# Kernel tuning notes

Hardware: AMD Instinct MI355X
Metric: run time of the kernel (lower is better)

## Reference

```python
import jax, jax.numpy as jnp
import numpy as np

N_NODES = 50000
N_EDGES = 800000
IN_DIM = 128
HID_DIM = 64
OUT_DIM = 40
N_REL = 8


def setup_inputs() -> dict:
    key = jax.random.key(0)
    ks = jax.random.split(key, 12)
    x = jax.random.normal(ks[0], (N_NODES, IN_DIM), dtype=jnp.float32)
    edge_index = jax.random.randint(ks[1], (2, N_EDGES), 0, N_NODES, dtype=jnp.int64)
    edge_type = jax.random.randint(ks[2], (N_EDGES,), 0, N_REL, dtype=jnp.int64)
    s = 0.05
    W1 = jax.random.normal(ks[3], (N_REL, IN_DIM, HID_DIM), dtype=jnp.float32) * s
    root1 = jax.random.normal(ks[4], (IN_DIM, HID_DIM), dtype=jnp.float32) * s
    b1 = jnp.zeros((HID_DIM,), dtype=jnp.float32)
    W2 = jax.random.normal(ks[5], (N_REL, HID_DIM, HID_DIM), dtype=jnp.float32) * s
    root2 = jax.random.normal(ks[6], (HID_DIM, HID_DIM), dtype=jnp.float32) * s
    b2 = jnp.zeros((HID_DIM,), dtype=jnp.float32)
    Wl = jax.random.normal(ks[7], (HID_DIM, OUT_DIM), dtype=jnp.float32) * s
    bl = jnp.zeros((OUT_DIM,), dtype=jnp.float32)
    return {"x": x, "edge_index": edge_index, "edge_type": edge_type,
            "W1": W1, "root1": root1, "b1": b1,
            "W2": W2, "root2": root2, "b2": b2,
            "Wl": Wl, "bl": bl}


def _rgcn_conv(x, W, Wroot, b, src, dst, edge_type):
    # PyG RGCNConv (no bases/blocks, aggr='mean'):
    #   out[i] = sum_r mean_{(j->i) of rel r} (x[j] @ W[r]) + x[i] @ Wroot + b
    N = x.shape[0]
    R = W.shape[0]
    h = jnp.einsum('ni,rio->rno', x, W)        # [R, N, out]
    msgs = h[edge_type, src]                   # [E, out] edge gather
    seg = edge_type * N + dst                  # per (relation, dst) segment
    sums = jax.ops.segment_sum(msgs, seg, num_segments=R * N)
    cnt = jax.ops.segment_sum(jnp.ones((msgs.shape[0],), x.dtype), seg,
                              num_segments=R * N)
    mean = sums / jnp.maximum(cnt, 1.0)[:, None]
    agg = mean.reshape(R, N, -1).sum(axis=0)   # sum over relations
    return agg + x @ Wroot + b


def reference(x, edge_index, edge_type, W1, root1, b1, W2, root2, b2, Wl, bl):
    src, dst = edge_index[0], edge_index[1]
    h = jax.nn.relu(_rgcn_conv(x, W1, root1, b1, src, dst, edge_type))
    # dropout is identity in eval mode
    h = jax.nn.relu(_rgcn_conv(h, W2, root2, b2, src, dst, edge_type))
    logits = h @ Wl + bl
    return jax.nn.log_softmax(logits, axis=1)
```

## Files before the change

### kernel.cpp

```cpp
#include <hip/hip_runtime.h>
#include <hip/hip_bf16.h>
#include <cmath>


#define IN_DIM 128
#define HID 64
#define OUT_DIM 40
#define NREL 8
#define NCOLS 576
#define CAP 64
#define CSTR 16

typedef __attribute__((ext_vector_type(8))) short short8;
typedef __attribute__((ext_vector_type(4))) short short4v;
typedef __attribute__((ext_vector_type(4))) float floatx4;
typedef __attribute__((ext_vector_type(2))) float f32x2;

static __device__ __forceinline__ short f2bf(float f) {
  __hip_bfloat16 h = __float2bfloat16(f);
  return __builtin_bit_cast(short, h);
}
static __device__ __forceinline__ float bflo(unsigned int u) {
  return __int_as_float(u << 16);
}
static __device__ __forceinline__ float bfhi(unsigned int u) {
  return __int_as_float(u & 0xffff0000u);
}
static __device__ __forceinline__ unsigned int packbf(float x, float y) {
  unsigned int lo = (unsigned short)f2bf(x);
  unsigned int hi = (unsigned short)f2bf(y);
  return lo | (hi << 16);
}

__global__ void pack_bt(const float* __restrict__ W1, const float* __restrict__ root1,
                        short* __restrict__ Bt1,
                        const float* __restrict__ W2, const float* __restrict__ root2,
                        short* __restrict__ Bt2,
                        int* __restrict__ cursor, int nzero4) {
  const int PB1 = (NCOLS * IN_DIM + 255) / 256;
  const int PB2 = (NCOLS * HID + 255) / 256;
  int b = blockIdx.x;
  if (b < PB1) {
    int i = b * 256 + threadIdx.x;
    if (i >= NCOLS * IN_DIM) return;
    int c = i / IN_DIM, k = i % IN_DIM;
    float v = (c < NREL * HID)
      ? W1[((size_t)(c >> 6) * IN_DIM + k) * HID + (c & 63)]
      : root1[(size_t)k * HID + (c - NREL * HID)];
    Bt1[i] = f2bf(v);
  } else if (b < PB1 + PB2) {
    int i = (b - PB1) * 256 + threadIdx.x;
    if (i >= NCOLS * HID) return;
    int c = i / HID, k = i % HID;
    float v = (c < NREL * HID)
      ? W2[((size_t)(c >> 6) * HID + k) * HID + (c & 63)]
      : root2[(size_t)k * HID + (c - NREL * HID)];
    Bt2[i] = f2bf(v);
  } else {
    int i = (b - PB1 - PB2) * 256 + threadIdx.x;
    if (i < nzero4) {
      int4 z; z.x = 0; z.y = 0; z.z = 0; z.w = 0;
      ((int4*)cursor)[i] = z;
    }
  }
}

template<int K, int AMODE>
__device__ __forceinline__ void gemm_dev(
    short* As, short* Bs,
    const void* __restrict__ Aptr, const short* __restrict__ Bt,
    const float* __restrict__ bias, short* __restrict__ H,
    unsigned short* __restrict__ AGG, int M, int row0)
{
  constexpr int AST = K + 8;
  constexpr int CB = K / 8;
  constexpr int NCH = 64 * CB / 256;
  int tid = threadIdx.x;
  int wv = tid >> 6, lane = tid & 63;
  int lm = lane & 15, quad = lane >> 4;

  int bn[NCH], bko[NCH];
  #pragma unroll
  for (int j = 0; j < NCH; ++j) {
    int i = tid + j * 256;
    bn[j] = i / CB; bko[j] = i % CB;
  }

  short8 breg[NCH];
  #pragma unroll
  for (int j = 0; j < NCH; ++j)
    breg[j] = *(const short8*)(Bt + (unsigned)(bn[j] * K + bko[j] * 8));

  if (AMODE == 0) {
    const float* A = (const float*)Aptr;
    constexpr int CH = K / 4;
    for (int i = tid; i < 64 * CH; i += 256) {
      int r = i / CH, kq = i % CH;
      int gr = row0 + r; if (gr >= M) gr = M - 1;
      float4 v = *(const float4*)(A + (unsigned)(gr * K + kq * 4));
      short4v s;
      s.x = f2bf(v.x); s.y = f2bf(v.y); s.z = f2bf(v.z); s.w = f2bf(v.w);
      *(short4v*)(As + r * AST + kq * 4) = s;
    }
  } else {
    const short* A = (const short*)Aptr;
    constexpr int CH = K / 8;
    for (int i = tid; i < 64 * CH; i += 256) {
      int r = i / CH, ko = i % CH;
      int gr = row0 + r; if (gr >= M) gr = M - 1;
      short8 v = *(const short8*)(A + (unsigned)(gr * K + ko * 8));
      #pragma unroll
      for (int j = 0; j < 8; ++j)
        if ((unsigned short)v[j] & 0x8000u) v[j] = 0;
      *(short8*)(As + r * AST + ko * 8) = v;
    }
  }

  const short* ap = As + (16 * wv + lm) * AST + quad * 8;
  int rowg = row0 + 16 * wv + lm;

  for (int cy = 0; cy < 9; ++cy) {
    #pragma unroll
    for (int j = 0; j < NCH; ++j)
      *(short8*)(Bs + bn[j] * AST + bko[j] * 8) = breg[j];
    __syncthreads();

    if (cy < 8) {
      #pragma unroll
      for (int j = 0; j < NCH; ++j)
        breg[j] = *(const short8*)(
            Bt + (unsigned)(((cy + 1) * 64 + bn[j]) * K + bko[j] * 8));
    }

    floatx4 acc[4] = {{0,0,0,0},{0,0,0,0},{0,0,0,0},{0,0,0,0}};
    #pragma unroll
    for (int ks = 0; ks < K / 32; ++ks) {
      short8 a = *(const short8*)(ap + ks * 32);
      #pragma unroll
      for (int nb = 0; nb < 4; ++nb) {
        short8 b = *(const short8*)(Bs + (nb * 16 + lm) * AST + ks * 32 + quad * 8);
        acc[nb] = __builtin_amdgcn_mfma_f32_16x16x32_bf16(b, a, acc[nb], 0, 0, 0);
      }
    }
    __syncthreads();

    if (cy < 8) {
      if (rowg < M) {
        short* hrow = H + (unsigned)rowg * (NREL * HID) + cy * 64 + quad * 4;
        #pragma unroll
        for (int nb = 0; nb < 4; ++nb) {
          short4v s;
          s.x = f2bf(acc[nb][0]); s.y = f2bf(acc[nb][1]);
          s.z = f2bf(acc[nb][2]); s.w = f2bf(acc[nb][3]);
          *(short4v*)(hrow + nb * 16) = s;
        }
      }
    } else {
      if (rowg < M) {
        unsigned short* arow = AGG + (unsigned)rowg * HID + quad * 4;
        #pragma unroll
        for (int nb = 0; nb < 4; ++nb) {
          float4 bv = *(const float4*)(bias + nb * 16 + quad * 4);
          short4v s;
          s.x = f2bf(acc[nb][0] + bv.x); s.y = f2bf(acc[nb][1] + bv.y);
          s.z = f2bf(acc[nb][2] + bv.z); s.w = f2bf(acc[nb][3] + bv.w);
          *(short4v*)(arow + nb * 16) = s;
        }
      }
    }
  }
}

__global__ __launch_bounds__(256, 4) void gemm1_scatter(
    const float* __restrict__ A, const short* __restrict__ Bt,
    const float* __restrict__ bias, short* __restrict__ H,
    unsigned short* __restrict__ AGG, int M, int SB,
    const int* __restrict__ src, const int* __restrict__ dst,
    const int* __restrict__ et,
    int* __restrict__ cursor, int* __restrict__ ev, int E)
{
  constexpr int AST = IN_DIM + 8;
  __shared__ short As[64 * AST];
  __shared__ short Bs[64 * AST];
  if ((int)blockIdx.x >= SB) {
    gemm_dev<IN_DIM, 0>(As, Bs, A, Bt, bias, H, AGG, M, (blockIdx.x - SB) * 64);
  } else {
    int e = blockIdx.x * 256 + threadIdx.x;
    if (e >= E) return;
    int d = dst[e];
    int pos = atomicAdd(&cursor[d * CSTR], 1);
    if (pos < CAP)
      __builtin_nontemporal_store((src[e] << 3) | et[e], &ev[d * CAP + pos]);
  }
}

__global__ __launch_bounds__(256, 4) void gemm2_mfma(
    const unsigned short* __restrict__ A, const short* __restrict__ Bt,
    const float* __restrict__ bias, short* __restrict__ H,
    unsigned short* __restrict__ AGG, int M)
{
  constexpr int AST = HID + 8;
  __shared__ short As[64 * AST];
  __shared__ short Bs[64 * AST];
  gemm_dev<HID, 1>(As, Bs, A, Bt, bias, H, AGG, M, blockIdx.x * 64);
}

static __device__ __forceinline__ void agg_dst(
    const uint2* __restrict__ Hu2, const int* __restrict__ evr,
    int4 e0, int4 e1, int4 e2, int4 e3,
    int cnt, int qloc, int sub, int lhl, int h,
    float& a0, float& a1, float& a2, float& a3)
{
  int vv0[8] = {e0.x, e0.y, e0.z, e0.w, e1.x, e1.y, e1.z, e1.w};
  int vv1[8] = {e2.x, e2.y, e2.z, e2.w, e3.x, e3.y, e3.z, e3.w};
  int base0 = qloc * 8, base1 = 16 + qloc * 8;
  uint2 hv[8];

  #pragma unroll
  for (int i = 0; i < 8; ++i) {
    bool ok = (base0 + i) < cnt;
    int v = ok ? vv0[i] : 0;
    hv[i] = Hu2[(unsigned)v * 16u + (unsigned)sub];
  }

  int myrel = lhl & 7;
  int c = 0;
  #pragma unroll
  for (int i = 0; i < 8; ++i)
    c += ((base0 + i) < cnt && (vv0[i] & 7) == myrel) ? 1 : 0;
  #pragma unroll
  for (int i = 0; i < 8; ++i)
    c += ((base1 + i) < cnt && (vv1[i] & 7) == myrel) ? 1 : 0;
  c += __shfl_xor(c, 16, 64);
  if (cnt > 32) {
    int eu = evr[32 + lhl];
    bool valid = (32 + lhl) < cnt;
    unsigned long long hm = 0xffffffffull << (h * 32);
    int rr = eu & 7;
    #pragma unroll
    for (int r = 0; r < 8; ++r) {
      unsigned long long m = __ballot(valid && rr == r);
      int cr = __popcll(m & hm);
      if (myrel == r) c += cr;
    }
  }
  float wreg = (c > 0) ? (1.0f / (float)c) : 0.0f;

  f32x2 A01 = {a0, a1}, A23 = {a2, a3};
  #pragma unroll
  for (int i = 0; i < 8; ++i) {
    bool ok = (base0 + i) < cnt;
    float w0 = __shfl(wreg, h * 32 + (vv0[i] & 7), 64);
    float w = ok ? w0 : 0.f;
    f32x2 w2 = {w, w};
    f32x2 h01 = {bflo(hv[i].x), bfhi(hv[i].x)};
    f32x2 h23 = {bflo(hv[i].y), bfhi(hv[i].y)};
    A01 += h01 * w2;
    A23 += h23 * w2;
  }
  if (cnt > 16) {
    #pragma unroll
    for (int i = 0; i < 8; ++i) {
      bool ok = (base1 + i) < cnt;
      int v = ok ? vv1[i] : 0;
      hv[i] = Hu2[(unsigned)v * 16u + (unsigned)sub];
    }
    #pragma unroll
    for (int i = 0; i < 8; ++i) {
      bool ok = (base1 + i) < cnt;
      float w0 = __shfl(wreg, h * 32 + (vv1[i] & 7), 64);
      float w = ok ? w0 : 0.f;
      f32x2 w2 = {w, w};
      f32x2 h01 = {bflo(hv[i].x), bfhi(hv[i].x)};
      f32x2 h23 = {bflo(hv[i].y), bfhi(hv[i].y)};
      A01 += h01 * w2;
      A23 += h23 * w2;
    }
  }
  if (cnt > 32) {
    #pragma unroll
    for (int P = 2; P < 4; ++P) {
      if (cnt > P * 16) {
        const int4* pp = (const int4*)(evr + P * 16 + qloc * 8);
        int4 f0 = pp[0], f1 = pp[1];
        int vv[8] = {f0.x, f0.y, f0.z, f0.w, f1.x, f1.y, f1.z, f1.w};
        int bs = P * 16 + qloc * 8;
        #pragma unroll
        for (int i = 0; i < 8; ++i) {
          bool ok = (bs + i) < cnt;
          int v = ok ? vv[i] : 0;
          hv[i] = Hu2[(unsigned)v * 16u + (unsigned)sub];
        }
        #pragma unroll
        for (int i = 0; i < 8; ++i) {
          bool ok = (bs + i) < cnt;
          float w0 = __shfl(wreg, h * 32 + (vv[i] & 7), 64);
          float w = ok ? w0 : 0.f;
          f32x2 w2 = {w, w};
          f32x2 h01 = {bflo(hv[i].x), bfhi(hv[i].x)};
          f32x2 h23 = {bflo(hv[i].y), bfhi(hv[i].y)};
          A01 += h01 * w2;
          A23 += h23 * w2;
        }
      }
    }
  }
  a0 = A01.x; a1 = A01.y; a2 = A23.x; a3 = A23.y;
  a0 += __shfl_xor(a0, 16, 64);
  a1 += __shfl_xor(a1, 16, 64);
  a2 += __shfl_xor(a2, 16, 64);
  a3 += __shfl_xor(a3, 16, 64);
}

__global__ __launch_bounds__(256) void csr_agg(
    const short* __restrict__ H, const int* __restrict__ cursor,
    const int* __restrict__ ev, unsigned short* __restrict__ AGG, int N)
{
  int tid = threadIdx.x;
  int wv = tid >> 6, lane = tid & 63;
  int h = lane >> 5, lhl = lane & 31, qloc = lhl >> 4, sub = lhl & 15;
  int d = blockIdx.x * 8 + wv * 2 + h;
  int dc = d < N ? d : N - 1;

  int cnt = cursor[dc * CSTR];
  const int* evr = ev + dc * CAP;
  const int4* p0 = (const int4*)(evr + qloc * 8);
  int4 e0 = p0[0], e1 = p0[1];
  const int4* p1 = (const int4*)(evr + 16 + qloc * 8);
  int4 e2 = p1[0], e3 = p1[1];
  uint2* aggrow = (uint2*)(AGG + (size_t)dc * HID);
  uint2 iv = {0, 0};
  if (qloc == 0) iv = aggrow[sub];
  if (cnt > CAP) cnt = CAP;

  float a0 = 0.f, a1 = 0.f, a2 = 0.f, a3 = 0.f;
  if (qloc == 0) {
    a0 = bflo(iv.x); a1 = bfhi(iv.x); a2 = bflo(iv.y); a3 = bfhi(iv.y);
  }
  agg_dst((const uint2*)H, evr, e0, e1, e2, e3, cnt, qloc, sub, lhl, h,
          a0, a1, a2, a3);
  if (d < N && qloc == 0) {
    uint2 ov;
    ov.x = packbf(a0, a1);
    ov.y = packbf(a2, a3);
    aggrow[sub] = ov;
  }
}

__global__ __launch_bounds__(256) void csr_agg_final(
    const short* __restrict__ H, const int* __restrict__ cursor,
    const int* __restrict__ ev, const unsigned short* __restrict__ AGG,
    const float* __restrict__ Wl, const float* __restrict__ bl,
    float* __restrict__ out, int N)
{
  __shared__ float sWl[HID * OUT_DIM];
  __shared__ float sbl[OUT_DIM];
  __shared__ float sh[8][HID];
  int tid = threadIdx.x;
  int wv = tid >> 6, lane = tid & 63;
  int h = lane >> 5, lhl = lane & 31, qloc = lhl >> 4, sub = lhl & 15;
  int d = blockIdx.x * 8 + wv * 2 + h;
  int dc = d < N ? d : N - 1;

  int cnt = cursor[dc * CSTR];
  const int* evr = ev + dc * CAP;
  const int4* p0 = (const int4*)(evr + qloc * 8);
  int4 e0 = p0[0], e1 = p0[1];
  const int4* p1 = (const int4*)(evr + 16 + qloc * 8);
  int4 e2 = p1[0], e3 = p1[1];
  uint2 iv = ((const uint2*)(AGG + (size_t)dc * HID))[sub];
  if (cnt > CAP) cnt = CAP;

  float a0 = 0.f, a1 = 0.f, a2 = 0.f, a3 = 0.f;
  if (qloc == 0) {
    a0 = bflo(iv.x); a1 = bfhi(iv.x); a2 = bflo(iv.y); a3 = bfhi(iv.y);
  }
  agg_dst((const uint2*)H, evr, e0, e1, e2, e3, cnt, qloc, sub, lhl, h,
          a0, a1, a2, a3);
  if (qloc == 0) {
    float4 v;
    v.x = fmaxf(a0, 0.f); v.y = fmaxf(a1, 0.f);
    v.z = fmaxf(a2, 0.f); v.w = fmaxf(a3, 0.f);
    *(float4*)(&sh[wv * 2 + h][4 * sub]) = v;
  }

  for (int i = tid; i < HID * OUT_DIM; i += 256) sWl[i] = Wl[i];
  if (tid < OUT_DIM) sbl[tid] = bl[tid];
  __syncthreads();

  #pragma unroll
  for (int ii = 0; ii < 2; ++ii) {
    int dd = blockIdx.x * 8 + wv * 2 + ii;
    const float* row = sh[wv * 2 + ii];
    float logit = -__builtin_inff();
    if (lane < OUT_DIM) {
      float t = sbl[lane];
      #pragma unroll 8
      for (int k = 0; k < HID; ++k) t += row[k] * sWl[k * OUT_DIM + lane];
      logit = t;
    }
    float m = logit;
    #pragma unroll
    for (int o = 32; o > 0; o >>= 1) m = fmaxf(m, __shfl_xor(m, o, 64));
    float ex = (lane < OUT_DIM) ? expf(logit - m) : 0.f;
    float s = ex;
    #pragma unroll
    for (int o = 32; o > 0; o >>= 1) s += __shfl_xor(s, o, 64);
    if (dd < N && lane < OUT_DIM)
      out[(size_t)dd * OUT_DIM + lane] = logit - m - logf(s);
  }
}

extern "C" void kernel_launch(void* const* d_in, const int* in_sizes, int n_in,
                              void* d_out, int out_size, void* d_ws, size_t ws_size,
                              hipStream_t stream) {
  const float* x     = (const float*)d_in[0];
  const int*   eidx  = (const int*)d_in[1];
  const int*   etype = (const int*)d_in[2];
  const float* W1    = (const float*)d_in[3];
  const float* root1 = (const float*)d_in[4];
  const float* b1    = (const float*)d_in[5];
  const float* W2    = (const float*)d_in[6];
  const float* root2 = (const float*)d_in[7];
  const float* b2    = (const float*)d_in[8];
  const float* Wl    = (const float*)d_in[9];
  const float* bl    = (const float*)d_in[10];

  int N = in_sizes[0] / IN_DIM;
  int E = in_sizes[2];
  const int* srcp = eidx;
  const int* dstp = eidx + E;

  char* ws = (char*)d_ws;
  size_t off = 0;
  auto alloc = [&](size_t bytes) -> char* {
    char* p = ws + off;
    off += (bytes + 255) & ~(size_t)255;
    return p;
  };
  short* Bt1    = (short*)alloc((size_t)NCOLS * IN_DIM * 2);
  short* Bt2    = (short*)alloc((size_t)NCOLS * HID * 2);
  int*   cursor = (int*)alloc((size_t)N * CSTR * 4);
  int*   ev     = (int*)alloc((size_t)N * CAP * 4);
  short* H1     = (short*)alloc((size_t)N * NREL * HID * 2);
  short* H2     = (short*)alloc((size_t)N * NREL * HID * 2);
  unsigned short* AGG1 = (unsigned short*)alloc((size_t)N * HID * 2);
  unsigned short* AGG2 = (unsigned short*)alloc((size_t)N * HID * 2);

  const int PB1 = (NCOLS * IN_DIM + 255) / 256;
  const int PB2 = (NCOLS * HID + 255) / 256;
  int nzero4 = (N * CSTR) / 4;
  int ZB = (nzero4 + 255) / 256;
  pack_bt<<<PB1 + PB2 + ZB, 256, 0, stream>>>(W1, root1, Bt1, W2, root2, Bt2,
                                              cursor, nzero4);

  int GB = (N + 63) / 64;
  int SB = (E + 255) / 256;
  gemm1_scatter<<<SB + GB, 256, 0, stream>>>(x, Bt1, b1, H1, AGG1, N, SB,
                                             srcp, dstp, etype, cursor, ev, E);

  csr_agg<<<(N + 7) / 8, 256, 0, stream>>>(H1, cursor, ev, AGG1, N);

  gemm2_mfma<<<GB, 256, 0, stream>>>(AGG1, Bt2, b2, H2, AGG2, N);

  csr_agg_final<<<(N + 7) / 8, 256, 0, stream>>>(H2, cursor, ev, AGG2,
                                                 Wl, bl, (float*)d_out, N);
}
```

Baseline: 266.4 us.

## Fuse layer-1 aggregation with layer-2 GEMM through shared memory

Merges the layer-1 CSR aggregation kernel and the layer-2 MFMA GEMM into one kernel. Each block aggregates 64 destination rows, applies ReLU, and writes them as bf16 straight into the GEMM's shared-memory A tile, so the AGG1 round trip through global memory and one launch go away. It also reorders gemm1_scatter so GEMM blocks come before scatter blocks in the grid. The cost is fewer concurrently active warps during aggregation (one block of 256 threads handles 64 rows serially in 8 reps) and more shared-memory pressure in the fused kernel.

```diff
diff --git a/kernel.cpp b/kernel.cpp
--- a/kernel.cpp
+++ b/kernel.cpp
@@ -91,7 +91,7 @@
   for (int j = 0; j < NCH; ++j)
     breg[j] = *(const short8*)(Bt + (unsigned)(bn[j] * K + bko[j] * 8));
 
-  if (AMODE == 0) {
+  if constexpr (AMODE == 0) {
     const float* A = (const float*)Aptr;
     constexpr int CH = K / 4;
     for (int i = tid; i < 64 * CH; i += 256) {
@@ -102,7 +102,7 @@
       s.x = f2bf(v.x); s.y = f2bf(v.y); s.z = f2bf(v.z); s.w = f2bf(v.w);
       *(short4v*)(As + r * AST + kq * 4) = s;
     }
-  } else {
+  } else if constexpr (AMODE == 1) {
     const short* A = (const short*)Aptr;
     constexpr int CH = K / 8;
     for (int i = tid; i < 64 * CH; i += 256) {
@@ -174,7 +174,7 @@
 __global__ __launch_bounds__(256, 4) void gemm1_scatter(
     const float* __restrict__ A, const short* __restrict__ Bt,
     const float* __restrict__ bias, short* __restrict__ H,
-    unsigned short* __restrict__ AGG, int M, int SB,
+    unsigned short* __restrict__ AGG, int M, int GB,
     const int* __restrict__ src, const int* __restrict__ dst,
     const int* __restrict__ et,
     int* __restrict__ cursor, int* __restrict__ ev, int E)
@@ -182,27 +182,16 @@
   constexpr int AST = IN_DIM + 8;
   __shared__ short As[64 * AST];
   __shared__ short Bs[64 * AST];
-  if ((int)blockIdx.x >= SB) {
-    gemm_dev<IN_DIM, 0>(As, Bs, A, Bt, bias, H, AGG, M, (blockIdx.x - SB) * 64);
+  if ((int)blockIdx.x < GB) {
+    gemm_dev<IN_DIM, 0>(As, Bs, A, Bt, bias, H, AGG, M, blockIdx.x * 64);
   } else {
-    int e = blockIdx.x * 256 + threadIdx.x;
+    int e = (blockIdx.x - GB) * 256 + threadIdx.x;
     if (e >= E) return;
     int d = dst[e];
     int pos = atomicAdd(&cursor[d * CSTR], 1);
     if (pos < CAP)
       __builtin_nontemporal_store((src[e] << 3) | et[e], &ev[d * CAP + pos]);
   }
-}
-
-__global__ __launch_bounds__(256, 4) void gemm2_mfma(
-    const unsigned short* __restrict__ A, const short* __restrict__ Bt,
-    const float* __restrict__ bias, short* __restrict__ H,
-    unsigned short* __restrict__ AGG, int M)
-{
-  constexpr int AST = HID + 8;
-  __shared__ short As[64 * AST];
-  __shared__ short Bs[64 * AST];
-  gemm_dev<HID, 1>(As, Bs, A, Bt, bias, H, AGG, M, blockIdx.x * 64);
 }
 
 static __device__ __forceinline__ void agg_dst(
@@ -312,39 +301,50 @@
   a3 += __shfl_xor(a3, 16, 64);
 }
 
-__global__ __launch_bounds__(256) void csr_agg(
-    const short* __restrict__ H, const int* __restrict__ cursor,
-    const int* __restrict__ ev, unsigned short* __restrict__ AGG, int N)
+__global__ __launch_bounds__(256) void agg_gemm2(
+    const short* __restrict__ H1, const int* __restrict__ cursor,
+    const int* __restrict__ ev, const unsigned short* __restrict__ AGG1,
+    const short* __restrict__ Bt2, const float* __restrict__ bias2,
+    short* __restrict__ H2, unsigned short* __restrict__ AGG2, int N)
 {
+  constexpr int AST = HID + 8;
+  __shared__ short As[64 * AST];
+  __shared__ short Bs[64 * AST];
   int tid = threadIdx.x;
   int wv = tid >> 6, lane = tid & 63;
   int h = lane >> 5, lhl = lane & 31, qloc = lhl >> 4, sub = lhl & 15;
-  int d = blockIdx.x * 8 + wv * 2 + h;
-  int dc = d < N ? d : N - 1;
-
-  int cnt = cursor[dc * CSTR];
-  const int* evr = ev + dc * CAP;
-  const int4* p0 = (const int4*)(evr + qloc * 8);
-  int4 e0 = p0[0], e1 = p0[1];
-  const int4* p1 = (const int4*)(evr + 16 + qloc * 8);
-  int4 e2 = p1[0], e3 = p1[1];
-  uint2* aggrow = (uint2*)(AGG + (size_t)dc * HID);
-  uint2 iv = {0, 0};
-  if (qloc == 0) iv = aggrow[sub];
-  if (cnt > CAP) cnt = CAP;
-
-  float a0 = 0.f, a1 = 0.f, a2 = 0.f, a3 = 0.f;
-  if (qloc == 0) {
-    a0 = bflo(iv.x); a1 = bfhi(iv.x); a2 = bflo(iv.y); a3 = bfhi(iv.y);
-  }
-  agg_dst((const uint2*)H, evr, e0, e1, e2, e3, cnt, qloc, sub, lhl, h,
-          a0, a1, a2, a3);
-  if (d < N && qloc == 0) {
-    uint2 ov;
-    ov.x = packbf(a0, a1);
-    ov.y = packbf(a2, a3);
-    aggrow[sub] = ov;
-  }
+  int hw = wv * 2 + h;
+  int row0 = blockIdx.x * 64;
+
+  for (int rep = 0; rep < 8; ++rep) {
+    int dloc = hw * 8 + rep;
+    int d = row0 + dloc;
+    int dc = d < N ? d : N - 1;
+
+    int cnt = cursor[dc * CSTR];
+    const int* evr = ev + dc * CAP;
+    const int4* p0 = (const int4*)(evr + qloc * 8);
+    int4 e0 = p0[0], e1 = p0[1];
+    const int4* p1 = (const int4*)(evr + 16 + qloc * 8);
+    int4 e2 = p1[0], e3 = p1[1];
+    uint2 iv = {0, 0};
+    if (qloc == 0) iv = ((const uint2*)(AGG1 + (size_t)dc * HID))[sub];
+    if (cnt > CAP) cnt = CAP;
+
+    float a0 = 0.f, a1 = 0.f, a2 = 0.f, a3 = 0.f;
+    if (qloc == 0) {
+      a0 = bflo(iv.x); a1 = bfhi(iv.x); a2 = bflo(iv.y); a3 = bfhi(iv.y);
+    }
+    agg_dst((const uint2*)H1, evr, e0, e1, e2, e3, cnt, qloc, sub, lhl, h,
+            a0, a1, a2, a3);
+    if (qloc == 0) {
+      short4v s;
+      s.x = f2bf(fmaxf(a0, 0.f)); s.y = f2bf(fmaxf(a1, 0.f));
+      s.z = f2bf(fmaxf(a2, 0.f)); s.w = f2bf(fmaxf(a3, 0.f));
+      *(short4v*)(As + dloc * AST + 4 * sub) = s;
+    }
+  }
+  gemm_dev<HID, 2>(As, Bs, nullptr, Bt2, bias2, H2, AGG2, N, row0);
 }
 
 __global__ __launch_bounds__(256) void csr_agg_final(
@@ -456,12 +456,11 @@
 
   int GB = (N + 63) / 64;
   int SB = (E + 255) / 256;
-  gemm1_scatter<<<SB + GB, 256, 0, stream>>>(x, Bt1, b1, H1, AGG1, N, SB,
+  gemm1_scatter<<<GB + SB, 256, 0, stream>>>(x, Bt1, b1, H1, AGG1, N, GB,
                                              srcp, dstp, etype, cursor, ev, E);
 
-  csr_agg<<<(N + 7) / 8, 256, 0, stream>>>(H1, cursor, ev, AGG1, N);
-
-  gemm2_mfma<<<GB, 256, 0, stream>>>(AGG1, Bt2, b2, H2, AGG2, N);
+  agg_gemm2<<<GB, 256, 0, stream>>>(H1, cursor, ev, AGG1, Bt2, b2,
+                                    H2, AGG2, N);
 
   csr_agg_final<<<(N + 7) / 8, 256, 0, stream>>>(H2, cursor, ev, AGG2,
                                                  Wl, bl, (float*)d_out, N);
```

Measured after the change: 249.6 us. -6.3%, faster.
